# Optimization experiments

Hardware: AMD Instinct MI355X
Metric: run time of the kernel (lower is better)

## Reference

```python
import jax, jax.numpy as jnp
import numpy as np

N = 33554432  # 2**25 elements
EPS = 1e-4    # keep probabilities strictly inside (0,1) to avoid log(0)

def setup_inputs() -> dict:
    key = jax.random.key(0)
    k1, k2 = jax.random.split(key)
    input_ = jax.random.uniform(k1, (N,), dtype=jnp.float32, minval=EPS, maxval=1.0 - EPS)
    target = jax.random.uniform(k2, (N,), dtype=jnp.float32, minval=EPS, maxval=1.0 - EPS)
    return {"input": input_, "target": target}

def reference(input, target):
    # Binary KL divergence per element, summed:
    # KL(p||q) = p*log(p/q) + (1-p)*log((1-p)/(1-q))
    p, q = input, target
    kl = p * (jnp.log(p) - jnp.log(q)) + (1.0 - p) * (jnp.log1p(-p) - jnp.log1p(-q))
    return kl.sum()
```

## Files before the change

### kernel.cpp

```cpp
#include <hip/hip_runtime.h>

#define BLOCK 256
#define GRID_FAST 8192
#define VPT   4

typedef float vfloat4 __attribute__((ext_vector_type(4)));

__device__ __forceinline__ void kl_acc(float p, float q, float& acc) {
    float omp = 1.0f - p;
    float omq = 1.0f - q;
    float d1  = __log2f(p)   - __log2f(q);
    float d2  = __log2f(omp) - __log2f(omq);
    acc = fmaf(p,   d1, acc);
    acc = fmaf(omp, d2, acc);
}

__device__ __forceinline__ void kl_acc4(vfloat4 pv, vfloat4 qv,
                                        float& a0, float& a1, float& a2, float& a3) {
    kl_acc(pv.x, qv.x, a0);
    kl_acc(pv.y, qv.y, a1);
    kl_acc(pv.z, qv.z, a2);
    kl_acc(pv.w, qv.w, a3);
}

__device__ __forceinline__ void block_reduce_and_atomic(float acc, float* out) {
    const float LN2 = 0.69314718055994530942f;
    #pragma unroll
    for (int off = 32; off > 0; off >>= 1)
        acc += __shfl_down(acc, off, 64);

    __shared__ float wave_sums[BLOCK / 64];
    const int lane = threadIdx.x & 63;
    const int wave = threadIdx.x >> 6;
    if (lane == 0) wave_sums[wave] = acc;
    __syncthreads();

    if (threadIdx.x == 0) {
        float s = 0.0f;
        #pragma unroll
        for (int w = 0; w < BLOCK / 64; ++w) s += wave_sums[w];
        atomicAdd(out, s * LN2);
    }
}

__global__ __launch_bounds__(BLOCK, 8) void kl_div_fast(
        const vfloat4* __restrict__ p4,
        const vfloat4* __restrict__ q4,
        float* __restrict__ out) {
    const int base = blockIdx.x * (BLOCK * VPT) + threadIdx.x;

    vfloat4 p0 = p4[base + 0 * BLOCK];
    vfloat4 p1 = p4[base + 1 * BLOCK];
    vfloat4 p2 = p4[base + 2 * BLOCK];
    vfloat4 p3 = p4[base + 3 * BLOCK];
    vfloat4 q0 = q4[base + 0 * BLOCK];
    vfloat4 q1 = q4[base + 1 * BLOCK];
    vfloat4 q2 = q4[base + 2 * BLOCK];
    vfloat4 q3 = q4[base + 3 * BLOCK];

    float a0 = 0.0f, a1 = 0.0f, a2 = 0.0f, a3 = 0.0f;
    kl_acc4(p0, q0, a0, a1, a2, a3);
    kl_acc4(p1, q1, a0, a1, a2, a3);
    kl_acc4(p2, q2, a0, a1, a2, a3);
    kl_acc4(p3, q3, a0, a1, a2, a3);

    float acc = (a0 + a1) + (a2 + a3);
    block_reduce_and_atomic(acc, out);
}

__global__ __launch_bounds__(BLOCK) void kl_div_generic(
        const float* __restrict__ p,
        const float* __restrict__ q,
        float* __restrict__ out,
        int n) {
    const int nvec = n >> 2;
    const vfloat4* __restrict__ p4 = reinterpret_cast<const vfloat4*>(p);
    const vfloat4* __restrict__ q4 = reinterpret_cast<const vfloat4*>(q);

    float acc = 0.0f;
    const int stride = gridDim.x * blockDim.x;
    for (int i = blockIdx.x * blockDim.x + threadIdx.x; i < nvec; i += stride) {
        vfloat4 pv = p4[i];
        vfloat4 qv = q4[i];
        kl_acc(pv.x, qv.x, acc);
        kl_acc(pv.y, qv.y, acc);
        kl_acc(pv.z, qv.z, acc);
        kl_acc(pv.w, qv.w, acc);
    }
    for (int i = (nvec << 2) + blockIdx.x * blockDim.x + threadIdx.x; i < n; i += stride) {
        kl_acc(p[i], q[i], acc);
    }
    block_reduce_and_atomic(acc, out);
}

extern "C" void kernel_launch(void* const* d_in, const int* in_sizes, int n_in,
                              void* d_out, int out_size, void* d_ws, size_t ws_size,
                              hipStream_t stream) {
    const float* p = (const float*)d_in[0];
    const float* q = (const float*)d_in[1];
    float* out = (float*)d_out;
    const int n = in_sizes[0];

    hipMemsetAsync(out, 0, sizeof(float), stream);

    if (n == GRID_FAST * BLOCK * VPT * 4) {
        kl_div_fast<<<GRID_FAST, BLOCK, 0, stream>>>(
            reinterpret_cast<const vfloat4*>(p),
            reinterpret_cast<const vfloat4*>(q), out);
    } else {
        kl_div_generic<<<2048, BLOCK, 0, stream>>>(p, q, out, n);
    }
}
```

Baseline: 296.9 us.

## Software-pipeline loads in grid-strided KL kernel with fewer, larger blocks

The fast path drops from 8192 blocks processing 4 vectors per thread to 2048 blocks processing 16 vectors per thread in a grid-strided pattern. Loads are double-buffered in batches of four, with the next batch issued before computing the current one, and sched_barrier keeps the compiler from reordering across stages. The aim is to hide memory latency per thread and cut atomics and block-launch overhead. In exchange, register pressure rises (launch bounds lowered to 4 waves), which may reduce occupancy.

```diff
diff --git a/kernel.cpp b/kernel.cpp
--- a/kernel.cpp
+++ b/kernel.cpp
@@ -1,8 +1,9 @@
 #include <hip/hip_runtime.h>
 
 #define BLOCK 256
-#define GRID_FAST 8192
-#define VPT   4
+#define GRID  2048
+#define VPT   16
+#define BATCH 4
 
 typedef float vfloat4 __attribute__((ext_vector_type(4)));
 
@@ -43,26 +44,41 @@
     }
 }
 
-__global__ __launch_bounds__(BLOCK, 8) void kl_div_fast(
+__global__ __launch_bounds__(BLOCK, 4) void kl_div_fast(
         const vfloat4* __restrict__ p4,
         const vfloat4* __restrict__ q4,
         float* __restrict__ out) {
-    const int base = blockIdx.x * (BLOCK * VPT) + threadIdx.x;
+    const int gid = blockIdx.x * BLOCK + threadIdx.x;
+    const int stride = GRID * BLOCK;
 
-    vfloat4 p0 = p4[base + 0 * BLOCK];
-    vfloat4 p1 = p4[base + 1 * BLOCK];
-    vfloat4 p2 = p4[base + 2 * BLOCK];
-    vfloat4 p3 = p4[base + 3 * BLOCK];
-    vfloat4 q0 = q4[base + 0 * BLOCK];
-    vfloat4 q1 = q4[base + 1 * BLOCK];
-    vfloat4 q2 = q4[base + 2 * BLOCK];
-    vfloat4 q3 = q4[base + 3 * BLOCK];
+    vfloat4 pc[BATCH], qc[BATCH];
+    #pragma unroll
+    for (int k = 0; k < BATCH; ++k) {
+        pc[k] = p4[gid + k * stride];
+        qc[k] = q4[gid + k * stride];
+    }
 
     float a0 = 0.0f, a1 = 0.0f, a2 = 0.0f, a3 = 0.0f;
-    kl_acc4(p0, q0, a0, a1, a2, a3);
-    kl_acc4(p1, q1, a0, a1, a2, a3);
-    kl_acc4(p2, q2, a0, a1, a2, a3);
-    kl_acc4(p3, q3, a0, a1, a2, a3);
+
+    #pragma unroll
+    for (int b = 1; b < VPT / BATCH; ++b) {
+        vfloat4 pn[BATCH], qn[BATCH];
+        #pragma unroll
+        for (int k = 0; k < BATCH; ++k) {
+            pn[k] = p4[gid + (b * BATCH + k) * stride];
+            qn[k] = q4[gid + (b * BATCH + k) * stride];
+        }
+        __builtin_amdgcn_sched_barrier(0);
+        #pragma unroll
+        for (int k = 0; k < BATCH; ++k)
+            kl_acc4(pc[k], qc[k], a0, a1, a2, a3);
+        #pragma unroll
+        for (int k = 0; k < BATCH; ++k) { pc[k] = pn[k]; qc[k] = qn[k]; }
+    }
+    __builtin_amdgcn_sched_barrier(0);
+    #pragma unroll
+    for (int k = 0; k < BATCH; ++k)
+        kl_acc4(pc[k], qc[k], a0, a1, a2, a3);
 
     float acc = (a0 + a1) + (a2 + a3);
     block_reduce_and_atomic(acc, out);
@@ -103,11 +119,11 @@
 
     hipMemsetAsync(out, 0, sizeof(float), stream);
 
-    if (n == GRID_FAST * BLOCK * VPT * 4) {
-        kl_div_fast<<<GRID_FAST, BLOCK, 0, stream>>>(
+    if (n == GRID * BLOCK * VPT * 4) {
+        kl_div_fast<<<GRID, BLOCK, 0, stream>>>(
             reinterpret_cast<const vfloat4*>(p),
             reinterpret_cast<const vfloat4*>(q), out);
     } else {
-        kl_div_generic<<<2048, BLOCK, 0, stream>>>(p, q, out, n);
+        kl_div_generic<<<GRID, BLOCK, 0, stream>>>(p, q, out, n);
     }
 }
```

Measured after the change: 277.7 us. -6.5%, faster.

## Stage inputs through double-buffered LDS with async global-to-LDS copies

Applied to the files above, without the earlier changes.

Replaces the one-shot register-load kernel with a persistent-style kernel. Each of 2048 blocks walks 8 stages of data. Inputs are copied straight into a double-buffered LDS tile with global_load_lds, so the next stage's load overlaps the current stage's log computations. The aim is better latency hiding and fewer blocks launched. The cost is extra LDS traffic, a barrier per stage and lower occupancy from the LDS footprint. Correctness also depends on the barrier waiting for the async copies to finish.

```diff
diff --git a/kernel.cpp b/kernel.cpp
--- a/kernel.cpp
+++ b/kernel.cpp
@@ -1,10 +1,18 @@
 #include <hip/hip_runtime.h>
 
-#define BLOCK 256
-#define GRID_FAST 8192
-#define VPT   4
+#define BLOCK  256
+#define GRID   2048
+#define S4     512
+#define STAGES 8
 
 typedef float vfloat4 __attribute__((ext_vector_type(4)));
+
+__device__ __forceinline__ void async_cp16(const vfloat4* g, vfloat4* lds_base) {
+    __builtin_amdgcn_global_load_lds(
+        (const __attribute__((address_space(1))) unsigned int*)g,
+        (__attribute__((address_space(3))) unsigned int*)lds_base,
+        16, 0, 0);
+}
 
 __device__ __forceinline__ void kl_acc(float p, float q, float& acc) {
     float omp = 1.0f - p;
@@ -43,26 +51,41 @@
     }
 }
 
-__global__ __launch_bounds__(BLOCK, 8) void kl_div_fast(
+__global__ __launch_bounds__(BLOCK, 4) void kl_div_lds(
         const vfloat4* __restrict__ p4,
         const vfloat4* __restrict__ q4,
         float* __restrict__ out) {
-    const int base = blockIdx.x * (BLOCK * VPT) + threadIdx.x;
+    __shared__ vfloat4 sp[2][S4];
+    __shared__ vfloat4 sq[2][S4];
 
-    vfloat4 p0 = p4[base + 0 * BLOCK];
-    vfloat4 p1 = p4[base + 1 * BLOCK];
-    vfloat4 p2 = p4[base + 2 * BLOCK];
-    vfloat4 p3 = p4[base + 3 * BLOCK];
-    vfloat4 q0 = q4[base + 0 * BLOCK];
-    vfloat4 q1 = q4[base + 1 * BLOCK];
-    vfloat4 q2 = q4[base + 2 * BLOCK];
-    vfloat4 q3 = q4[base + 3 * BLOCK];
+    const int t    = threadIdx.x;
+    const int w    = t >> 6;
+    const int lane = t & 63;
+    const size_t base = (size_t)blockIdx.x * (S4 * STAGES);
 
+    auto stage = [&](int s, int buf) {
+        const size_t g0 = base + (size_t)s * S4 + w * 128 + lane;
+        async_cp16(p4 + g0,      &sp[buf][w * 128]);
+        async_cp16(p4 + g0 + 64, &sp[buf][w * 128 + 64]);
+        async_cp16(q4 + g0,      &sq[buf][w * 128]);
+        async_cp16(q4 + g0 + 64, &sq[buf][w * 128 + 64]);
+    };
+
+    stage(0, 0);
     float a0 = 0.0f, a1 = 0.0f, a2 = 0.0f, a3 = 0.0f;
-    kl_acc4(p0, q0, a0, a1, a2, a3);
-    kl_acc4(p1, q1, a0, a1, a2, a3);
-    kl_acc4(p2, q2, a0, a1, a2, a3);
-    kl_acc4(p3, q3, a0, a1, a2, a3);
+
+    #pragma unroll
+    for (int s = 0; s < STAGES; ++s) {
+        const int buf = s & 1;
+        __syncthreads();
+        if (s + 1 < STAGES) stage(s + 1, buf ^ 1);
+        vfloat4 pv0 = sp[buf][t];
+        vfloat4 qv0 = sq[buf][t];
+        vfloat4 pv1 = sp[buf][t + 256];
+        vfloat4 qv1 = sq[buf][t + 256];
+        kl_acc4(pv0, qv0, a0, a1, a2, a3);
+        kl_acc4(pv1, qv1, a0, a1, a2, a3);
+    }
 
     float acc = (a0 + a1) + (a2 + a3);
     block_reduce_and_atomic(acc, out);
@@ -103,11 +126,11 @@
 
     hipMemsetAsync(out, 0, sizeof(float), stream);
 
-    if (n == GRID_FAST * BLOCK * VPT * 4) {
-        kl_div_fast<<<GRID_FAST, BLOCK, 0, stream>>>(
+    if (n == GRID * S4 * STAGES * 4) {
+        kl_div_lds<<<GRID, BLOCK, 0, stream>>>(
             reinterpret_cast<const vfloat4*>(p),
             reinterpret_cast<const vfloat4*>(q), out);
     } else {
-        kl_div_generic<<<2048, BLOCK, 0, stream>>>(p, q, out, n);
+        kl_div_generic<<<GRID, BLOCK, 0, stream>>>(p, q, out, n);
     }
 }
```

Measured after the change: 279.6 us. -5.8%, faster.
